# Kernel tuning notes

Hardware: AMD Instinct MI355X
Metric: run time of the kernel (lower is better)

The kernel has to match this reference:

```python
import jax, jax.numpy as jnp
import numpy as np

KERNEL_MUL = 2.0
KERNEL_NUM = 5


def _mmd(source, target):
    n = source.shape[0]
    total = jnp.concatenate([source, target], axis=0)          # [2N, D]
    n_samples = total.shape[0]
    # GEMM-based pairwise squared L2 distances (same math as broadcast subtract/square/sum)
    sq = jnp.sum(total * total, axis=-1)                        # [2N]
    L2 = sq[:, None] + sq[None, :] - 2.0 * (total @ total.T)    # [2N, 2N]
    # bandwidth from detached distances (torch uses .data)
    bw = jax.lax.stop_gradient(jnp.sum(L2)) / (n_samples ** 2 - n_samples)
    bw = bw / (KERNEL_MUL ** (KERNEL_NUM // 2))
    kernels = jnp.zeros_like(L2)
    for i in range(KERNEL_NUM):
        kernels = kernels + jnp.exp(-L2 / (bw * KERNEL_MUL ** i))
    XX = kernels[:n, :n]
    YY = kernels[n:, n:]
    XY = kernels[:n, n:]
    YX = kernels[n:, :n]
    return jnp.mean(XX + YY - XY - YX)


def setup_inputs() -> dict:
    key = jax.random.key(0)
    k1, k2 = jax.random.split(key)
    N, D = 4096, 128
    source = jax.random.normal(k1, (N, D), dtype=jnp.float32)
    target = jax.random.normal(k2, (N, D), dtype=jnp.float32)
    return {"source": source, "target": target}


def reference(source, target):
    return _mmd(source, target)
```

## Files before the change

### kernel.cpp

```cpp
#include <hip/hip_runtime.h>

#define D 128
#define NT2 2080
#define NPART 8320

typedef __attribute__((ext_vector_type(8))) short short8;
typedef __attribute__((ext_vector_type(4))) float float4v;
typedef __attribute__((ext_vector_type(2))) float float2v;

static __device__ __forceinline__ unsigned short f2bf(float f) {
    unsigned int u = __float_as_uint(f);
    unsigned int r = (u + 0x7fffu + ((u >> 16) & 1u)) >> 16;
    return (unsigned short)r;
}

static __device__ __forceinline__ void gld16(const void* g, void* l) {
    __builtin_amdgcn_global_load_lds(
        (const __attribute__((address_space(1))) unsigned int*)g,
        (__attribute__((address_space(3))) unsigned int*)l, 16, 0, 0);
}


__global__ __launch_bounds__(256) void k_prep(const float* __restrict__ src,
                                              const float* __restrict__ tgt,
                                              float* __restrict__ wsf,
                                              unsigned int* __restrict__ XTu) {
    if (blockIdx.x < 2048) {
        float* rowsq = wsf + 33280;
        const int wv = threadIdx.x >> 6, lane = threadIdx.x & 63;
        const int gr = blockIdx.x * 4 + wv;
        const float* Xr = (gr < 4096) ? src + (size_t)gr * D : tgt + (size_t)(gr - 4096) * D;
        float2 f = ((const float2*)Xr)[lane];
        XTu[(gr >> 4) * 1024 + (lane >> 2) * 64 + (gr & 15) * 4 + (lane & 3)] =
            (unsigned)f2bf(f.x) | ((unsigned)f2bf(f.y) << 16);
        float s = f.x * f.x + f.y * f.y;
        #pragma unroll
        for (int off = 32; off; off >>= 1) s += __shfl_down(s, off);
        if (lane == 0) rowsq[gr] = s;
    } else {
        float* colpart = wsf + 512;
        int b = blockIdx.x - 2048;
        int col = threadIdx.x & 127, half = threadIdx.x >> 7;
        const float* X = (b < 64) ? src + (size_t)(b * 64) * D
                                  : tgt + (size_t)((b - 64) * 64) * D;
        float p0 = 0.f, p1 = 0.f, p2 = 0.f, p3 = 0.f;
        #pragma unroll 4
        for (int i = 0; i < 32; i += 4) {
            p0 += X[(size_t)(2 * (i + 0) + half) * D + col];
            p1 += X[(size_t)(2 * (i + 1) + half) * D + col];
            p2 += X[(size_t)(2 * (i + 2) + half) * D + col];
            p3 += X[(size_t)(2 * (i + 3) + half) * D + col];
        }
        __shared__ float cp[2][128];
        cp[half][col] = (p0 + p1) + (p2 + p3);
        __syncthreads();
        if (threadIdx.x < 128)
            colpart[b * 128 + threadIdx.x] = cp[0][threadIdx.x] + cp[1][threadIdx.x];
    }
}

__global__ __launch_bounds__(256) void p3_consts(float* __restrict__ wsf) {
    const float* colpart = wsf + 512;
    const float* rowsq = wsf + 33280;
    const int tid = threadIdx.x, lane = tid & 63;

    float s0 = 0.f, s1 = 0.f, s2 = 0.f, s3 = 0.f;
    #pragma unroll
    for (int i = 0; i < 32; i += 4) {
        s0 += rowsq[tid + 256 * (i + 0)];
        s1 += rowsq[tid + 256 * (i + 1)];
        s2 += rowsq[tid + 256 * (i + 2)];
        s3 += rowsq[tid + 256 * (i + 3)];
    }
    float s = (s0 + s1) + (s2 + s3);
    #pragma unroll
    for (int off = 32; off; off >>= 1) s += __shfl_down(s, off);
    __shared__ float red[8];
    __shared__ float csum[128];
    if (lane == 0) red[tid >> 6] = s;

    int c = tid & 127, h = tid >> 7;
    float q0 = 0.f, q1 = 0.f, q2 = 0.f, q3 = 0.f;
    #pragma unroll 4
    for (int b = 0; b < 64; b += 4) {
        q0 += colpart[(h * 64 + b + 0) * 128 + c];
        q1 += colpart[(h * 64 + b + 1) * 128 + c];
        q2 += colpart[(h * 64 + b + 2) * 128 + c];
        q3 += colpart[(h * 64 + b + 3) * 128 + c];
    }
    float cs = (q0 + q1) + (q2 + q3);
    __syncthreads();
    if (h == 0) csum[c] = cs;
    __syncthreads();
    if (h == 1) csum[c] += cs;
    __syncthreads();
    float v = (tid < 128) ? csum[tid] * csum[tid] : 0.f;
    #pragma unroll
    for (int off = 32; off; off >>= 1) v += __shfl_down(v, off);
    if (lane == 0) red[4 + (tid >> 6)] = v;
    __syncthreads();
    if (tid == 0) {
        double ss = (double)red[0] + red[1] + red[2] + red[3];
        double s2 = (double)red[4] + red[5] + red[6] + red[7];
        double sumL2 = 2.0 * 8192.0 * ss - 2.0 * s2;
        double bw = sumL2 / (8192.0 * 8192.0 - 8192.0) / 4.0;
        wsf[4] = (float)(-1.4426950408889634 / (bw * 16.0));
    }
}

__global__ __launch_bounds__(256) void mmd_main(const uint4* __restrict__ XT,
                                                const float* __restrict__ wsf,
                                                float* __restrict__ partial) {
    __shared__ uint4 lds[4096];
    const float* rowsq = wsf + 33280;
    const int tid = threadIdx.x;
    const int lane = tid & 63, wv = tid >> 6;
    const int quad = lane >> 4, mrow = lane & 15;
    const int wm = wv >> 1, wn = wv & 1;

    int b = blockIdx.x;
    int t2 = (b & 7) * (NT2 / 8) + (b >> 3);

    int pi = (int)((129.0 - sqrt(129.0 * 129.0 - 8.0 * (double)t2)) * 0.5);
    auto base = [](int p) { return (p * (129 - p)) >> 1; };
    while (base(pi + 1) <= t2) ++pi;
    while (base(pi) > t2) --pi;
    int pj = pi + (t2 - base(pi));

    const char* gA = (const char*)(XT + (size_t)pi * 2048);
    char* lb = (char*)lds;
    #pragma unroll
    for (int it = 0; it < 8; ++it)
        gld16(gA + it * 4096 + tid * 16, lb + it * 4096 + tid * 16);
    if (pj != pi) {
        const char* gB = (const char*)(XT + (size_t)pj * 2048);
        #pragma unroll
        for (int it = 0; it < 8; ++it)
            gld16(gB + it * 4096 + tid * 16, lb + 32768 + it * 4096 + tid * 16);
    }
    const uint4* As = lds + wm * 1024;
    const uint4* Bs = ((pj != pi) ? lds + 2048 : lds) + wn * 1024;
    const int ti = pi * 2 + wm, tj = pj * 2 + wn;
    float c4 = wsf[4];
    __syncthreads();

    float4v acc[4][4];
    #pragma unroll
    for (int mt = 0; mt < 4; ++mt)
        #pragma unroll
        for (int nt = 0; nt < 4; ++nt)
            acc[mt][nt] = (float4v){0.f, 0.f, 0.f, 0.f};

    #pragma unroll
    for (int kc = 0; kc < 4; ++kc) {
        short8 af[4], bf[4];
        #pragma unroll
        for (int mt = 0; mt < 4; ++mt)
            af[mt] = *(const short8*)&As[mt * 256 + kc * 64 + lane];
        #pragma unroll
        for (int nt = 0; nt < 4; ++nt)
            bf[nt] = *(const short8*)&Bs[nt * 256 + kc * 64 + lane];
        #pragma unroll
        for (int mt = 0; mt < 4; ++mt)
            #pragma unroll
            for (int nt = 0; nt < 4; ++nt)
                acc[mt][nt] = __builtin_amdgcn_mfma_f32_16x16x32_bf16(af[mt], bf[nt], acc[mt][nt], 0, 0, 0);
    }

    const float* rsqA = rowsq + ti * 64;
    const float* rsqB = rowsq + tj * 64;
    const float cm2 = -2.f * c4;
    const float2v cm2v = {cm2, cm2};
    float2v part2 = {0.f, 0.f};
    #pragma unroll
    for (int mt = 0; mt < 4; ++mt) {
        const float2v rA01 = { rsqA[mt * 16 + quad * 4 + 0] * c4,
                               rsqA[mt * 16 + quad * 4 + 1] * c4 };
        const float2v rA23 = { rsqA[mt * 16 + quad * 4 + 2] * c4,
                               rsqA[mt * 16 + quad * 4 + 3] * c4 };
        #pragma unroll
        for (int nt = 0; nt < 4; ++nt) {
            float rBc = rsqB[nt * 16 + mrow] * c4;
            const float2v rB2 = {rBc, rBc};
            float4v d = acc[mt][nt];
            float2v d01 = {d[0], d[1]}, d23 = {d[2], d[3]};
            float2v a01 = d01 * cm2v + (rA01 + rB2);
            float2v a23 = d23 * cm2v + (rA23 + rB2);
            float2v e1a = { __builtin_amdgcn_exp2f(a01[0]), __builtin_amdgcn_exp2f(a01[1]) };
            float2v e1b = { __builtin_amdgcn_exp2f(a23[0]), __builtin_amdgcn_exp2f(a23[1]) };
            float2v e2a = e1a * e1a, e4a = e2a * e2a, e8a = e4a * e4a, e16a = e8a * e8a;
            float2v e2b = e1b * e1b, e4b = e2b * e2b, e8b = e4b * e4b, e16b = e8b * e8b;
            part2 += (e1a + e2a) + ((e4a + e8a) + e16a);
            part2 += (e1b + e2b) + ((e4b + e8b) + e16b);
        }
    }
    float part = part2[0] + part2[1];
    #pragma unroll
    for (int off = 32; off; off >>= 1) part += __shfl_down(part, off);

    if (lane == 0) {
        float wgt;
        if (pi == pj) {
            if (wm == 1 && wn == 0) wgt = 0.f;
            else wgt = (ti == tj) ? 1.f : 2.f;
        } else {
            wgt = ((pi < 32) == (pj < 32)) ? 2.f : -2.f;
        }
        partial[t2 * 4 + wv] = wgt * part;
    }
}

__global__ __launch_bounds__(256) void f_final(const float* __restrict__ wsf,
                                               float* __restrict__ out) {
    const float* partial = wsf + 41472;
    int tid = threadIdx.x, lane = tid & 63;
    double a0 = 0.0, a1 = 0.0, a2 = 0.0, a3 = 0.0;
    #pragma unroll 4
    for (int i = tid; i < NPART; i += 1024) {
        a0 += (double)partial[i];
        if (i + 256 < NPART) a1 += (double)partial[i + 256];
        if (i + 512 < NPART) a2 += (double)partial[i + 512];
        if (i + 768 < NPART) a3 += (double)partial[i + 768];
    }
    double s = (a0 + a1) + (a2 + a3);
    #pragma unroll
    for (int off = 32; off; off >>= 1) s += __shfl_down(s, off);
    __shared__ double r4[4];
    if (lane == 0) r4[tid >> 6] = s;
    __syncthreads();
    if (tid == 0)
        out[0] = (float)(((r4[0] + r4[1]) + (r4[2] + r4[3])) * (1.0 / (4096.0 * 4096.0)));
}

extern "C" void kernel_launch(void* const* d_in, const int* in_sizes, int n_in,
                              void* d_out, int out_size, void* d_ws, size_t ws_size,
                              hipStream_t stream) {
    const float* src = (const float*)d_in[0];
    const float* tgt = (const float*)d_in[1];
    float* wsf = (float*)d_ws;
    unsigned int* XTu = (unsigned int*)(wsf + 65536);
    float* partial = wsf + 41472;

    hipLaunchKernelGGL(k_prep, dim3(2176), dim3(256), 0, stream, src, tgt, wsf, XTu);
    hipLaunchKernelGGL(p3_consts, dim3(1), dim3(256), 0, stream, wsf);
    hipLaunchKernelGGL(mmd_main, dim3(NT2), dim3(256), 0, stream,
                       (const uint4*)XTu, wsf, partial);
    hipLaunchKernelGGL(f_final, dim3(1), dim3(256), 0, stream, wsf, (float*)d_out);
}
```

Baseline: 93.11 us.

## Fold constant and final reduction kernels into prep and main via atomics

Drops the single-block p3_consts and f_final kernels. k_prep now accumulates row-norm sums and column sums with atomics into 32 and 128 slots. Each mmd_main block recomputes the bandwidth constant from those slots, and the last block, found with a completion counter, reduces 32 double accumulators and writes the output. A memset is added to zero the accumulators. This removes two serial single-block launches and their tail latency, at the cost of atomic contention and float atomics that may give nondeterministic rounding.

```diff
diff --git a/kernel.cpp b/kernel.cpp
--- a/kernel.cpp
+++ b/kernel.cpp
@@ -2,7 +2,6 @@
 
 #define D 128
 #define NT2 2080
-#define NPART 8320
 
 typedef __attribute__((ext_vector_type(8))) short short8;
 typedef __attribute__((ext_vector_type(4))) float float4v;
@@ -25,6 +24,8 @@
                                               const float* __restrict__ tgt,
                                               float* __restrict__ wsf,
                                               unsigned int* __restrict__ XTu) {
+    __shared__ float shs[4];
+    __shared__ float cp[2][128];
     if (blockIdx.x < 2048) {
         float* rowsq = wsf + 33280;
         const int wv = threadIdx.x >> 6, lane = threadIdx.x & 63;
@@ -36,9 +37,11 @@
         float s = f.x * f.x + f.y * f.y;
         #pragma unroll
         for (int off = 32; off; off >>= 1) s += __shfl_down(s, off);
-        if (lane == 0) rowsq[gr] = s;
+        if (lane == 0) { rowsq[gr] = s; shs[wv] = s; }
+        __syncthreads();
+        if (threadIdx.x == 0)
+            atomicAdd(wsf + 8 + (blockIdx.x & 31), (shs[0] + shs[1]) + (shs[2] + shs[3]));
     } else {
-        float* colpart = wsf + 512;
         int b = blockIdx.x - 2048;
         int col = threadIdx.x & 127, half = threadIdx.x >> 7;
         const float* X = (b < 64) ? src + (size_t)(b * 64) * D
@@ -51,73 +54,43 @@
             p2 += X[(size_t)(2 * (i + 2) + half) * D + col];
             p3 += X[(size_t)(2 * (i + 3) + half) * D + col];
         }
-        __shared__ float cp[2][128];
         cp[half][col] = (p0 + p1) + (p2 + p3);
         __syncthreads();
         if (threadIdx.x < 128)
-            colpart[b * 128 + threadIdx.x] = cp[0][threadIdx.x] + cp[1][threadIdx.x];
-    }
-}
-
-__global__ __launch_bounds__(256) void p3_consts(float* __restrict__ wsf) {
-    const float* colpart = wsf + 512;
-    const float* rowsq = wsf + 33280;
-    const int tid = threadIdx.x, lane = tid & 63;
-
-    float s0 = 0.f, s1 = 0.f, s2 = 0.f, s3 = 0.f;
-    #pragma unroll
-    for (int i = 0; i < 32; i += 4) {
-        s0 += rowsq[tid + 256 * (i + 0)];
-        s1 += rowsq[tid + 256 * (i + 1)];
-        s2 += rowsq[tid + 256 * (i + 2)];
-        s3 += rowsq[tid + 256 * (i + 3)];
-    }
-    float s = (s0 + s1) + (s2 + s3);
-    #pragma unroll
-    for (int off = 32; off; off >>= 1) s += __shfl_down(s, off);
-    __shared__ float red[8];
-    __shared__ float csum[128];
-    if (lane == 0) red[tid >> 6] = s;
-
-    int c = tid & 127, h = tid >> 7;
-    float q0 = 0.f, q1 = 0.f, q2 = 0.f, q3 = 0.f;
-    #pragma unroll 4
-    for (int b = 0; b < 64; b += 4) {
-        q0 += colpart[(h * 64 + b + 0) * 128 + c];
-        q1 += colpart[(h * 64 + b + 1) * 128 + c];
-        q2 += colpart[(h * 64 + b + 2) * 128 + c];
-        q3 += colpart[(h * 64 + b + 3) * 128 + c];
-    }
-    float cs = (q0 + q1) + (q2 + q3);
-    __syncthreads();
-    if (h == 0) csum[c] = cs;
-    __syncthreads();
-    if (h == 1) csum[c] += cs;
-    __syncthreads();
-    float v = (tid < 128) ? csum[tid] * csum[tid] : 0.f;
-    #pragma unroll
-    for (int off = 32; off; off >>= 1) v += __shfl_down(v, off);
-    if (lane == 0) red[4 + (tid >> 6)] = v;
-    __syncthreads();
-    if (tid == 0) {
-        double ss = (double)red[0] + red[1] + red[2] + red[3];
-        double s2 = (double)red[4] + red[5] + red[6] + red[7];
-        double sumL2 = 2.0 * 8192.0 * ss - 2.0 * s2;
-        double bw = sumL2 / (8192.0 * 8192.0 - 8192.0) / 4.0;
-        wsf[4] = (float)(-1.4426950408889634 / (bw * 16.0));
+            atomicAdd(wsf + 64 + threadIdx.x, cp[0][threadIdx.x] + cp[1][threadIdx.x]);
     }
 }
 
 __global__ __launch_bounds__(256) void mmd_main(const uint4* __restrict__ XT,
-                                                const float* __restrict__ wsf,
-                                                float* __restrict__ partial) {
+                                                float* __restrict__ wsf,
+                                                float* __restrict__ out) {
     __shared__ uint4 lds[4096];
+    __shared__ float fpart[4];
+    __shared__ int lastflag;
     const float* rowsq = wsf + 33280;
     const int tid = threadIdx.x;
     const int lane = tid & 63, wv = tid >> 6;
     const int quad = lane >> 4, mrow = lane & 15;
     const int wm = wv >> 1, wn = wv & 1;
 
+    float c4;
+    {
+        const float* colsum = wsf + 64;
+        const float* ss32 = wsf + 8;
+        float cA = colsum[lane], cB = colsum[64 + lane];
+        float sq = cA * cA + cB * cB;
+        float sv = (lane < 32) ? ss32[lane] : 0.f;
+        #pragma unroll
+        for (int off = 32; off; off >>= 1) {
+            sq += __shfl_down(sq, off);
+            sv += __shfl_down(sv, off);
+        }
+        double sumL2 = 2.0 * 8192.0 * (double)sv - 2.0 * (double)sq;
+        double bw = sumL2 / (8192.0 * 8192.0 - 8192.0) / 4.0;
+        float c4l = (float)(-1.4426950408889634 / (bw * 16.0));
+        c4 = __shfl(c4l, 0);
+    }
+
     int b = blockIdx.x;
     int t2 = (b & 7) * (NT2 / 8) + (b >> 3);
 
@@ -141,7 +114,6 @@
     const uint4* As = lds + wm * 1024;
     const uint4* Bs = ((pj != pi) ? lds + 2048 : lds) + wn * 1024;
     const int ti = pi * 2 + wm, tj = pj * 2 + wn;
-    float c4 = wsf[4];
     __syncthreads();
 
     float4v acc[4][4];
@@ -206,30 +178,25 @@
         } else {
             wgt = ((pi < 32) == (pj < 32)) ? 2.f : -2.f;
         }
-        partial[t2 * 4 + wv] = wgt * part;
-    }
-}
-
-__global__ __launch_bounds__(256) void f_final(const float* __restrict__ wsf,
-                                               float* __restrict__ out) {
-    const float* partial = wsf + 41472;
-    int tid = threadIdx.x, lane = tid & 63;
-    double a0 = 0.0, a1 = 0.0, a2 = 0.0, a3 = 0.0;
-    #pragma unroll 4
-    for (int i = tid; i < NPART; i += 1024) {
-        a0 += (double)partial[i];
-        if (i + 256 < NPART) a1 += (double)partial[i + 256];
-        if (i + 512 < NPART) a2 += (double)partial[i + 512];
-        if (i + 768 < NPART) a3 += (double)partial[i + 768];
-    }
-    double s = (a0 + a1) + (a2 + a3);
-    #pragma unroll
-    for (int off = 32; off; off >>= 1) s += __shfl_down(s, off);
-    __shared__ double r4[4];
-    if (lane == 0) r4[tid >> 6] = s;
+        fpart[wv] = wgt * part;
+    }
     __syncthreads();
-    if (tid == 0)
-        out[0] = (float)(((r4[0] + r4[1]) + (r4[2] + r4[3])) * (1.0 / (4096.0 * 4096.0)));
+    if (tid == 0) {
+        double bs = ((double)fpart[0] + fpart[1]) + ((double)fpart[2] + fpart[3]);
+        double* accd = (double*)(wsf + 192);
+        atomicAdd(accd + (b & 31), bs);
+        asm volatile("s_waitcnt vmcnt(0)" ::: "memory");
+        unsigned int old = atomicAdd((unsigned int*)wsf, 1u);
+        lastflag = (old == NT2 - 1) ? 1 : 0;
+    }
+    __syncthreads();
+    if (lastflag && wv == 0) {
+        double* accd = (double*)(wsf + 192);
+        double v = (lane < 32) ? atomicAdd(accd + lane, 0.0) : 0.0;
+        #pragma unroll
+        for (int off = 32; off; off >>= 1) v += __shfl_down(v, off);
+        if (lane == 0) out[0] = (float)(v * (1.0 / (4096.0 * 4096.0)));
+    }
 }
 
 extern "C" void kernel_launch(void* const* d_in, const int* in_sizes, int n_in,
@@ -239,11 +206,9 @@
     const float* tgt = (const float*)d_in[1];
     float* wsf = (float*)d_ws;
     unsigned int* XTu = (unsigned int*)(wsf + 65536);
-    float* partial = wsf + 41472;
-
+
+    hipMemsetAsync(wsf, 0, 1024, stream);
     hipLaunchKernelGGL(k_prep, dim3(2176), dim3(256), 0, stream, src, tgt, wsf, XTu);
-    hipLaunchKernelGGL(p3_consts, dim3(1), dim3(256), 0, stream, wsf);
     hipLaunchKernelGGL(mmd_main, dim3(NT2), dim3(256), 0, stream,
-                       (const uint4*)XTu, wsf, partial);
-    hipLaunchKernelGGL(f_final, dim3(1), dim3(256), 0, stream, wsf, (float*)d_out);
-}
+                       (const uint4*)XTu, wsf, (float*)d_out);
+}
```

New measurement: 135.9 us. 45.9% more time.
